# Kernel optimization log

Measured on AMD Instinct MI355X. Metric: run time of the kernel, lower is better.

Reference implementation:

```python
import jax, jax.numpy as jnp
import numpy as np


def setup_inputs() -> dict:
    key = jax.random.key(0)
    # batch of 1D signals; DST is applied along the last dimension
    x = jax.random.normal(key, (16384, 1024), dtype=jnp.float32)
    return {"x": x}


def reference(x):
    # DST-II: y_k = sum_{n=0}^{N-1} x_n * sin(pi/N * (n + 1/2) * (k + 1))
    # (The original docstring says 'cos' but the op is a discrete SINE transform;
    #  the DREAMPlace kernel computes the DST-II above via FFT-style tricks.)
    N = x.shape[-1]
    n = jnp.arange(N, dtype=x.dtype)
    k = jnp.arange(N, dtype=x.dtype)
    # [N, N] sine basis: rows indexed by n (input), cols by k (output)
    S = jnp.sin((jnp.pi / N) * (n[:, None] + 0.5) * (k[None, :] + 1.0))
    # batched transform over leading dims
    lead = x.shape[:-1]
    y = jnp.einsum('bn,nk->bk', x.reshape(-1, N), S)
    return y.reshape(*lead, N)
```

## Files before the change

### kernel.cpp

```cpp
#include <hip/hip_runtime.h>
#include <cstdint>


static constexpr int BR4[16] = {0, 8, 4, 12, 2, 10, 6, 14,
                                1, 9, 5, 13, 3, 11, 7, 15};
static constexpr float W16C[8] = {1.0f, 0.9238795325f, 0.7071067812f,
                                  0.3826834324f, 0.0f, -0.3826834324f,
                                  -0.7071067812f, -0.9238795325f};
static constexpr float W16S[8] = {-0.0f, -0.3826834324f, -0.7071067812f,
                                  -0.9238795325f, -1.0f, -0.9238795325f,
                                  -0.7071067812f, -0.3826834324f};

__device__ __forceinline__ float sinr(float r) {
  return __builtin_amdgcn_sinf(r);
}
__device__ __forceinline__ float cosr(float r) {
  float t = r + 0.25f;
  t -= (t >= 1.0f) ? 1.0f : 0.0f;
  return __builtin_amdgcn_sinf(t);
}

__device__ __forceinline__ void twmul(int tw, float xr, float xi,
                                      float& yr, float& yi) {
  if (tw == 0) {
    yr = xr; yi = xi;
  } else if (tw == 4) {
    yr = xi; yi = -xr;
  } else if (tw == 2) {
    yr = 0.70710678118f * (xr + xi);
    yi = 0.70710678118f * (xi - xr);
  } else if (tw == 6) {
    yr = 0.70710678118f * (xi - xr);
    yi = -0.70710678118f * (xr + xi);
  } else {
    yr = xr * W16C[tw] - xi * W16S[tw];
    yi = xr * W16S[tw] + xi * W16C[tw];
  }
}

__global__ __launch_bounds__(256, 2) void dst_fft(const float* __restrict__ X,
                                                  float* __restrict__ Y) {
  __shared__ __align__(16) float lds_all[4][64 * 16];

  const int t = threadIdx.x;
  const int l = t & 63;
  const int w = t >> 6;
  float* lds = &lds_all[w][0];
  const int wid = blockIdx.x * 4 + w;

  const int c = l & 3;
  const int m2l = l >> 2;
  const int e = ((c & 1) << 1) | (c >> 1);
  const int sstar = (int)(__brev((unsigned)m2l) >> 28);
  const int pl = sstar >> 3;
  const int ccs = (sstar >> 1) & 3;
  const int subo = (sstar & 1) * 2;

  float2 ld[2][8];
  {
    const float* xr = X + (size_t)(wid * 2) * 1024;
#pragma unroll
    for (int j = 0; j < 8; ++j)
      ld[0][j] = *(const float2*)(xr + 2 * l + 128 * j);
  }

#pragma unroll
  for (int it = 0; it < 2; ++it) {
    const int row = wid * 2 + it;

    float re[16], im[16], odd[8];
#pragma unroll
    for (int j = 0; j < 8; ++j) {
      re[j] = ld[it][j].x;
      odd[j] = ld[it][j].y;
    }
#pragma unroll
    for (int j = 0; j < 8; ++j)
      re[15 - j] = -__shfl_xor(odd[j], 63);

#pragma unroll
    for (int o = 0; o < 8; ++o) {
      float d = re[o] - re[o + 8];
      re[o] += re[o + 8];
      im[o] = 0.0f;
      if (o == 0) {
        re[8] = d;            im[8] = 0.0f;
      } else if (o == 4) {
        re[12] = 0.0f;        im[12] = -d;
      } else {
        re[o + 8] = d * W16C[o];
        im[o + 8] = d * W16S[o];
      }
    }
#pragma unroll
    for (int H = 4; H >= 1; H >>= 1) {
#pragma unroll
      for (int b = 0; b < 16; b += 2 * H) {
#pragma unroll
        for (int o = 0; o < H; ++o) {
          int i0 = b + o, i1 = i0 + H;
          float ar = re[i0] - re[i1], ai = im[i0] - im[i1];
          re[i0] += re[i1];
          im[i0] += im[i1];
          twmul(o * (8 / H), ar, ai, re[i1], im[i1]);
        }
      }
    }

    {
      float rb = (float)l * (1.0f / 1024.0f);
      float wr = cosr(rb), wi = -sinr(rb);
      float cr = wr, ci = wi;
#pragma unroll
      for (int m2 = 1; m2 < 16; ++m2) {
        if (m2 > 1) {
          float nr = cr * wr - ci * wi;
          ci = cr * wi + ci * wr;
          cr = nr;
        }
        int i = BR4[m2];
        float tr = re[i] * cr - im[i] * ci;
        im[i] = re[i] * ci + im[i] * cr;
        re[i] = tr;
      }
    }

    float re2[16], im2[16];
#pragma unroll
    for (int p = 0; p < 2; ++p) {
      __asm__ volatile("s_waitcnt lgkmcnt(0)" ::: "memory");
#pragma unroll
      for (int cc = 0; cc < 4; ++cc) {
        int ch = 4 * p + cc;
        float4 v = make_float4(re[2 * ch], im[2 * ch],
                               re[2 * ch + 1], im[2 * ch + 1]);
        *(float4*)(lds + l * 16 + ((cc ^ ((l >> 1) & 3)) & 3) * 4) = v;
      }
      __asm__ volatile("s_waitcnt lgkmcnt(0)" ::: "memory");
      if (pl == p) {
#pragma unroll
        for (int i = 0; i < 16; ++i) {
          int r = c + 4 * BR4[i];
          int q = (ccs ^ ((r >> 1) & 3)) & 3;
          float2 v = *(const float2*)(lds + r * 16 + q * 4 + subo);
          re2[i] = v.x;
          im2[i] = v.y;
        }
      }
    }

    if (it == 0) {
      const float* xr1 = X + (size_t)(wid * 2 + 1) * 1024;
#pragma unroll
      for (int j = 0; j < 8; ++j)
        ld[1][j] = *(const float2*)(xr1 + 2 * l + 128 * j);
    }

#pragma unroll
    for (int H = 1; H <= 8; H <<= 1) {
#pragma unroll
      for (int b = 0; b < 16; b += 2 * H) {
#pragma unroll
        for (int o = 0; o < H; ++o) {
          int i0 = b + o, i1 = i0 + H;
          float tr, ti;
          twmul(o * (8 / H), re2[i1], im2[i1], tr, ti);
          re2[i1] = re2[i0] - tr;
          im2[i1] = im2[i0] - ti;
          re2[i0] += tr;
          im2[i0] += ti;
        }
      }
    }

    {
      float rb = (float)c * (1.0f / 64.0f);
      float br = cosr(rb), bi = -sinr(rb);
      float cr = br, ci = bi;
#pragma unroll
      for (int m = 1; m < 16; ++m) {
        if (m > 1) {
          float nr = cr * br - ci * bi;
          ci = cr * bi + ci * br;
          cr = nr;
        }
        float tr = re2[m] * cr - im2[m] * ci;
        im2[m] = re2[m] * ci + im2[m] * cr;
        re2[m] = tr;
      }
    }

    {
      const float sgA = (c & 2) ? -1.0f : 1.0f;
      const bool rot = (c == 3);
      const float sgB = (c & 1) ? -1.0f : 1.0f;
#pragma unroll
      for (int i = 0; i < 16; ++i) {
        float tr = __shfl_xor(re2[i], 2), ti = __shfl_xor(im2[i], 2);
        float ar = tr + sgA * re2[i], ai = ti + sgA * im2[i];
        float br = rot ? ai : ar;
        float bi = rot ? -ar : ai;
        tr = __shfl_xor(br, 1);
        ti = __shfl_xor(bi, 1);
        re2[i] = tr + sgB * br;
        im2[i] = ti + sgB * bi;
      }
    }

    {
      const float DC = 0.99969881869620422f;
      const float DS = 0.02454122852291229f;
      float r0 = (float)(m2l + 256 * e) * (1.0f / 4096.0f);
      float pc = cosr(r0), ps = sinr(r0);
      float* yr = Y + (size_t)row * 1024 + (1023 - m2l - 256 * e);
#pragma unroll
      for (int s2 = 0; s2 < 16; ++s2) {
        yr[-16 * s2] = re2[s2] * pc + im2[s2] * ps;
        if (s2 < 15) {
          float nc = pc * DC - ps * DS;
          ps = ps * DC + pc * DS;
          pc = nc;
        }
      }
    }
  }
}

extern "C" void kernel_launch(void* const* d_in, const int* in_sizes, int n_in,
                              void* d_out, int out_size, void* d_ws, size_t ws_size,
                              hipStream_t stream) {
  const float* X = (const float*)d_in[0];
  float* Y = (float*)d_out;
  dst_fft<<<dim3(2048), dim3(256), 0, stream>>>(X, Y);
}
```

Baseline: 124.7 us.

## Pack two real rows into one complex FFT and split with Hermitian symmetry

Instead of running two separate half-real FFTs, one for each row, the kernel loads both rows up front and places row A in the real part and row B in the imaginary part of a single 1024-point complex FFT. It then separates the two spectra with conjugate-symmetric pairing (X[k] and conj X[N-k]), exchanged through LDS, before applying the DST post-twiddle. This roughly halves the butterfly and twiddle arithmetic per row pair. In exchange it adds two LDS round trips, more complex index and swizzle logic, and a larger live register set from holding both rows' loads at once.

```diff
diff --git a/kernel.cpp b/kernel.cpp
--- a/kernel.cpp
+++ b/kernel.cpp
@@ -47,6 +47,7 @@
   const int w = t >> 6;
   float* lds = &lds_all[w][0];
   const int wid = blockIdx.x * 4 + w;
+  const int rowA = wid * 2;
 
   const int c = l & 3;
   const int m2l = l >> 2;
@@ -56,172 +57,207 @@
   const int ccs = (sstar >> 1) & 3;
   const int subo = (sstar & 1) * 2;
 
-  float2 ld[2][8];
-  {
-    const float* xr = X + (size_t)(wid * 2) * 1024;
-#pragma unroll
-    for (int j = 0; j < 8; ++j)
-      ld[0][j] = *(const float2*)(xr + 2 * l + 128 * j);
-  }
-
-#pragma unroll
-  for (int it = 0; it < 2; ++it) {
-    const int row = wid * 2 + it;
-
-    float re[16], im[16], odd[8];
-#pragma unroll
-    for (int j = 0; j < 8; ++j) {
-      re[j] = ld[it][j].x;
-      odd[j] = ld[it][j].y;
-    }
-#pragma unroll
-    for (int j = 0; j < 8; ++j)
-      re[15 - j] = -__shfl_xor(odd[j], 63);
-
-#pragma unroll
-    for (int o = 0; o < 8; ++o) {
-      float d = re[o] - re[o + 8];
-      re[o] += re[o + 8];
-      im[o] = 0.0f;
-      if (o == 0) {
-        re[8] = d;            im[8] = 0.0f;
-      } else if (o == 4) {
-        re[12] = 0.0f;        im[12] = -d;
+  const int Lp = (3 - c) + 4 * ((16 - m2l) & 15);
+  const int Lp0 = (c < 2) ? c : (5 - c);
+  const int pb = (m2l == 0) ? 16 : 15;
+  const int swzP = (Lp >> 1) & 3;
+  const int swzP0 = (Lp0 >> 1) & 3;
+
+  const float* xa = X + (size_t)rowA * 1024;
+  float2 la[8], lb[8];
+#pragma unroll
+  for (int j = 0; j < 8; ++j) la[j] = *(const float2*)(xa + 2 * l + 128 * j);
+#pragma unroll
+  for (int j = 0; j < 8; ++j)
+    lb[j] = *(const float2*)(xa + 1024 + 2 * l + 128 * j);
+
+  float re[16], im[16];
+#pragma unroll
+  for (int j = 0; j < 8; ++j) re[j] = la[j].x;
+#pragma unroll
+  for (int j = 0; j < 8; ++j) re[15 - j] = -__shfl_xor(la[j].y, 63);
+#pragma unroll
+  for (int j = 0; j < 8; ++j) im[j] = lb[j].x;
+#pragma unroll
+  for (int j = 0; j < 8; ++j) im[15 - j] = -__shfl_xor(lb[j].y, 63);
+
+#pragma unroll
+  for (int H = 8; H >= 1; H >>= 1) {
+#pragma unroll
+    for (int b = 0; b < 16; b += 2 * H) {
+#pragma unroll
+      for (int o = 0; o < H; ++o) {
+        int i0 = b + o, i1 = i0 + H;
+        float ar = re[i0] - re[i1], ai = im[i0] - im[i1];
+        re[i0] += re[i1];
+        im[i0] += im[i1];
+        twmul(o * (8 / H), ar, ai, re[i1], im[i1]);
+      }
+    }
+  }
+
+  {
+    float rb = (float)l * (1.0f / 1024.0f);
+    float wr = cosr(rb), wi = -sinr(rb);
+    float cr = wr, ci = wi;
+#pragma unroll
+    for (int m2 = 1; m2 < 16; ++m2) {
+      if (m2 > 1) {
+        float nr = cr * wr - ci * wi;
+        ci = cr * wi + ci * wr;
+        cr = nr;
+      }
+      int i = BR4[m2];
+      float tr = re[i] * cr - im[i] * ci;
+      im[i] = re[i] * ci + im[i] * cr;
+      re[i] = tr;
+    }
+  }
+
+  float re2[16], im2[16];
+#pragma unroll
+  for (int p = 0; p < 2; ++p) {
+    if (p)
+      __asm__ volatile("s_waitcnt lgkmcnt(0)" ::: "memory");
+#pragma unroll
+    for (int cc = 0; cc < 4; ++cc) {
+      int ch = 4 * p + cc;
+      float4 v = make_float4(re[2 * ch], im[2 * ch],
+                             re[2 * ch + 1], im[2 * ch + 1]);
+      *(float4*)(lds + l * 16 + ((cc ^ ((l >> 1) & 3)) & 3) * 4) = v;
+    }
+    __asm__ volatile("s_waitcnt lgkmcnt(0)" ::: "memory");
+    if (pl == p) {
+#pragma unroll
+      for (int i = 0; i < 16; ++i) {
+        int r = c + 4 * BR4[i];
+        int q = (ccs ^ ((r >> 1) & 3)) & 3;
+        float2 v = *(const float2*)(lds + r * 16 + q * 4 + subo);
+        re2[i] = v.x;
+        im2[i] = v.y;
+      }
+    }
+  }
+
+#pragma unroll
+  for (int H = 1; H <= 8; H <<= 1) {
+#pragma unroll
+    for (int b = 0; b < 16; b += 2 * H) {
+#pragma unroll
+      for (int o = 0; o < H; ++o) {
+        int i0 = b + o, i1 = i0 + H;
+        float tr, ti;
+        twmul(o * (8 / H), re2[i1], im2[i1], tr, ti);
+        re2[i1] = re2[i0] - tr;
+        im2[i1] = im2[i0] - ti;
+        re2[i0] += tr;
+        im2[i0] += ti;
+      }
+    }
+  }
+
+  {
+    float rb = (float)c * (1.0f / 64.0f);
+    float br = cosr(rb), bi = -sinr(rb);
+    float cr = br, ci = bi;
+#pragma unroll
+    for (int m = 1; m < 16; ++m) {
+      if (m > 1) {
+        float nr = cr * br - ci * bi;
+        ci = cr * bi + ci * br;
+        cr = nr;
+      }
+      float tr = re2[m] * cr - im2[m] * ci;
+      im2[m] = re2[m] * ci + im2[m] * cr;
+      re2[m] = tr;
+    }
+  }
+
+  {
+    const float sgA = (c & 2) ? -1.0f : 1.0f;
+    const bool rot = (c == 3);
+    const float sgB = (c & 1) ? -1.0f : 1.0f;
+#pragma unroll
+    for (int i = 0; i < 16; ++i) {
+      float tr = __shfl_xor(re2[i], 2), ti = __shfl_xor(im2[i], 2);
+      float ar = tr + sgA * re2[i], ai = ti + sgA * im2[i];
+      float br = rot ? ai : ar;
+      float bi = rot ? -ar : ai;
+      tr = __shfl_xor(br, 1);
+      ti = __shfl_xor(bi, 1);
+      re2[i] = tr + sgB * br;
+      im2[i] = ti + sgB * bi;
+    }
+  }
+
+  const float DC = 0.99969881869620422f;
+  const float DS = 0.02454122852291229f;
+  float r15 = (float)(m2l + 240 + 256 * e) * (1.0f / 4096.0f);
+  float pcd = cosr(r15), psd = sinr(r15);
+  float r0 = (float)(m2l + 256 * e) * (1.0f / 4096.0f);
+  float pc0 = cosr(r0), ps0 = sinr(r0);
+  float* ya = Y + (size_t)rowA * 1024 + (1023 - m2l - 256 * e);
+  float* yb = ya + 1024;
+
+  __asm__ volatile("s_waitcnt lgkmcnt(0)" ::: "memory");
+#pragma unroll
+  for (int cc = 0; cc < 4; ++cc) {
+    float4 v = make_float4(re2[2 * cc], im2[2 * cc],
+                           re2[2 * cc + 1], im2[2 * cc + 1]);
+    *(float4*)(lds + l * 16 + ((cc ^ ((l >> 1) & 3)) & 3) * 4) = v;
+  }
+  __asm__ volatile("s_waitcnt lgkmcnt(0)" ::: "memory");
+#pragma unroll
+  for (int s2 = 15; s2 >= 8; --s2) {
+    int q = (pb - s2) & 7;
+    float2 Q = *(const float2*)(lds + Lp * 16 + (((q >> 1) ^ swzP) & 3) * 4 +
+                                (q & 1) * 2);
+    float oa = 0.5f * ((re2[s2] + Q.x) * pcd + (im2[s2] - Q.y) * psd);
+    float ob = 0.5f * ((im2[s2] + Q.y) * pcd + (Q.x - re2[s2]) * psd);
+    if (s2 == 8) {
+      if (m2l != 0) { ya[-16 * s2] = oa; yb[-16 * s2] = ob; }
+    } else {
+      ya[-16 * s2] = oa;
+      yb[-16 * s2] = ob;
+    }
+    float nc = pcd * DC + psd * DS;
+    psd = psd * DC - pcd * DS;
+    pcd = nc;
+  }
+  if (m2l == 0) {
+    float2 Q = *(const float2*)(lds + Lp0 * 16 + ((0 ^ swzP0) & 3) * 4);
+    ya[0] = 0.5f * ((re2[0] + Q.x) * pc0 + (im2[0] - Q.y) * ps0);
+    yb[0] = 0.5f * ((im2[0] + Q.y) * pc0 + (Q.x - re2[0]) * ps0);
+  }
+
+  __asm__ volatile("s_waitcnt lgkmcnt(0)" ::: "memory");
+#pragma unroll
+  for (int cc = 0; cc < 4; ++cc) {
+    float4 v = make_float4(re2[8 + 2 * cc], im2[8 + 2 * cc],
+                           re2[9 + 2 * cc], im2[9 + 2 * cc]);
+    *(float4*)(lds + l * 16 + ((cc ^ ((l >> 1) & 3)) & 3) * 4) = v;
+  }
+  __asm__ volatile("s_waitcnt lgkmcnt(0)" ::: "memory");
+  {
+    float pca = pc0, psa = ps0;
+#pragma unroll
+    for (int s2 = 0; s2 <= 8; ++s2) {
+      int q = (((pb - s2) & 15) - 8) & 7;
+      float2 Q = *(const float2*)(lds + Lp * 16 + (((q >> 1) ^ swzP) & 3) * 4 +
+                                  (q & 1) * 2);
+      float oa = 0.5f * ((re2[s2] + Q.x) * pca + (im2[s2] - Q.y) * psa);
+      float ob = 0.5f * ((im2[s2] + Q.y) * pca + (Q.x - re2[s2]) * psa);
+      if (s2 == 0) {
+        if (m2l != 0) { ya[0] = oa; yb[0] = ob; }
+      } else if (s2 == 8) {
+        if (m2l == 0) { ya[-16 * 8] = oa; yb[-16 * 8] = ob; }
       } else {
-        re[o + 8] = d * W16C[o];
-        im[o + 8] = d * W16S[o];
-      }
-    }
-#pragma unroll
-    for (int H = 4; H >= 1; H >>= 1) {
-#pragma unroll
-      for (int b = 0; b < 16; b += 2 * H) {
-#pragma unroll
-        for (int o = 0; o < H; ++o) {
-          int i0 = b + o, i1 = i0 + H;
-          float ar = re[i0] - re[i1], ai = im[i0] - im[i1];
-          re[i0] += re[i1];
-          im[i0] += im[i1];
-          twmul(o * (8 / H), ar, ai, re[i1], im[i1]);
-        }
-      }
-    }
-
-    {
-      float rb = (float)l * (1.0f / 1024.0f);
-      float wr = cosr(rb), wi = -sinr(rb);
-      float cr = wr, ci = wi;
-#pragma unroll
-      for (int m2 = 1; m2 < 16; ++m2) {
-        if (m2 > 1) {
-          float nr = cr * wr - ci * wi;
-          ci = cr * wi + ci * wr;
-          cr = nr;
-        }
-        int i = BR4[m2];
-        float tr = re[i] * cr - im[i] * ci;
-        im[i] = re[i] * ci + im[i] * cr;
-        re[i] = tr;
-      }
-    }
-
-    float re2[16], im2[16];
-#pragma unroll
-    for (int p = 0; p < 2; ++p) {
-      __asm__ volatile("s_waitcnt lgkmcnt(0)" ::: "memory");
-#pragma unroll
-      for (int cc = 0; cc < 4; ++cc) {
-        int ch = 4 * p + cc;
-        float4 v = make_float4(re[2 * ch], im[2 * ch],
-                               re[2 * ch + 1], im[2 * ch + 1]);
-        *(float4*)(lds + l * 16 + ((cc ^ ((l >> 1) & 3)) & 3) * 4) = v;
-      }
-      __asm__ volatile("s_waitcnt lgkmcnt(0)" ::: "memory");
-      if (pl == p) {
-#pragma unroll
-        for (int i = 0; i < 16; ++i) {
-          int r = c + 4 * BR4[i];
-          int q = (ccs ^ ((r >> 1) & 3)) & 3;
-          float2 v = *(const float2*)(lds + r * 16 + q * 4 + subo);
-          re2[i] = v.x;
-          im2[i] = v.y;
-        }
-      }
-    }
-
-    if (it == 0) {
-      const float* xr1 = X + (size_t)(wid * 2 + 1) * 1024;
-#pragma unroll
-      for (int j = 0; j < 8; ++j)
-        ld[1][j] = *(const float2*)(xr1 + 2 * l + 128 * j);
-    }
-
-#pragma unroll
-    for (int H = 1; H <= 8; H <<= 1) {
-#pragma unroll
-      for (int b = 0; b < 16; b += 2 * H) {
-#pragma unroll
-        for (int o = 0; o < H; ++o) {
-          int i0 = b + o, i1 = i0 + H;
-          float tr, ti;
-          twmul(o * (8 / H), re2[i1], im2[i1], tr, ti);
-          re2[i1] = re2[i0] - tr;
-          im2[i1] = im2[i0] - ti;
-          re2[i0] += tr;
-          im2[i0] += ti;
-        }
-      }
-    }
-
-    {
-      float rb = (float)c * (1.0f / 64.0f);
-      float br = cosr(rb), bi = -sinr(rb);
-      float cr = br, ci = bi;
-#pragma unroll
-      for (int m = 1; m < 16; ++m) {
-        if (m > 1) {
-          float nr = cr * br - ci * bi;
-          ci = cr * bi + ci * br;
-          cr = nr;
-        }
-        float tr = re2[m] * cr - im2[m] * ci;
-        im2[m] = re2[m] * ci + im2[m] * cr;
-        re2[m] = tr;
-      }
-    }
-
-    {
-      const float sgA = (c & 2) ? -1.0f : 1.0f;
-      const bool rot = (c == 3);
-      const float sgB = (c & 1) ? -1.0f : 1.0f;
-#pragma unroll
-      for (int i = 0; i < 16; ++i) {
-        float tr = __shfl_xor(re2[i], 2), ti = __shfl_xor(im2[i], 2);
-        float ar = tr + sgA * re2[i], ai = ti + sgA * im2[i];
-        float br = rot ? ai : ar;
-        float bi = rot ? -ar : ai;
-        tr = __shfl_xor(br, 1);
-        ti = __shfl_xor(bi, 1);
-        re2[i] = tr + sgB * br;
-        im2[i] = ti + sgB * bi;
-      }
-    }
-
-    {
-      const float DC = 0.99969881869620422f;
-      const float DS = 0.02454122852291229f;
-      float r0 = (float)(m2l + 256 * e) * (1.0f / 4096.0f);
-      float pc = cosr(r0), ps = sinr(r0);
-      float* yr = Y + (size_t)row * 1024 + (1023 - m2l - 256 * e);
-#pragma unroll
-      for (int s2 = 0; s2 < 16; ++s2) {
-        yr[-16 * s2] = re2[s2] * pc + im2[s2] * ps;
-        if (s2 < 15) {
-          float nc = pc * DC - ps * DS;
-          ps = ps * DC + pc * DS;
-          pc = nc;
-        }
-      }
+        ya[-16 * s2] = oa;
+        yb[-16 * s2] = ob;
+      }
+      float nc = pca * DC - psa * DS;
+      psa = psa * DC + pca * DS;
+      pca = nc;
     }
   }
 }
```

Result: faster. 114.1 us (-8.5%).
